# Performance work log

Measured on AMD Instinct MI355X. Metric: run time of the kernel, lower is better.

Reference implementation:

```python
import jax, jax.numpy as jnp
import numpy as np

B, S, H, NSPAN = 16, 1024, 768, 5
NEG_INF = -1e9


def setup_inputs() -> dict:
    key = jax.random.key(0)
    k1, k2, k3, k4, k5, k6 = jax.random.split(key, 6)
    hidden = jax.random.normal(k1, (B, S, H), dtype=jnp.float32)
    full_emb = jax.random.normal(k2, (B, H), dtype=jnp.float32)
    # nn.Linear weights [out,in] per span head, plus biases and queries
    attn_W = jax.random.normal(k3, (NSPAN, H, H), dtype=jnp.float32) / np.sqrt(H)
    attn_b = jax.random.normal(k4, (NSPAN, H), dtype=jnp.float32) * 0.02
    attn_q = jax.random.uniform(k5, (NSPAN, H), dtype=jnp.float32)  # torch.rand init
    spans = jnp.sort(jax.random.randint(k6, (B, NSPAN, 2), 0, S), axis=-1)
    return {"hidden": hidden, "full_emb": full_emb, "attn_W": attn_W,
            "attn_b": attn_b, "attn_q": attn_q, "spans": spans}


def reference(hidden, full_emb, attn_W, attn_b, attn_q, spans):
    b, s, h = hidden.shape
    starts = spans[..., 0]            # [B,J]
    ends = spans[..., 1]              # [B,J]
    pos = jnp.arange(s)
    mask = (pos[None, None, :] >= starts[..., None]) & (pos[None, None, :] < ends[..., None])  # [B,J,S]
    count = mask.sum(-1)              # [B,J]
    fmask = mask.astype(hidden.dtype)

    # mean pool over each span (zeros when start==end)
    mean = jnp.einsum('bjs,bsh->bjh', fmask, hidden) / jnp.maximum(count, 1).astype(hidden.dtype)[..., None]

    # learned attention pool: tanh(Linear_j(words)), scores vs query_j, softmax over span
    proj = jnp.tanh(jnp.einsum('bsh,joh->bjso', hidden, attn_W) + attn_b[None, :, None, :])  # [B,J,S,H]
    scores = jnp.einsum('jo,bjso->bjs', attn_q, proj)
    scores = jnp.where(mask, scores, NEG_INF)  # max-subtraction in original is a detached shift => identical
    alphas = jax.nn.softmax(scores, axis=-1)
    att = jnp.einsum('bjs,bsh->bjh', alphas, hidden)

    nonempty = (count > 0)[..., None]
    mean = jnp.where(nonempty, mean, 0.0)
    att = jnp.where(nonempty, att, 0.0)

    span_reps = jnp.concatenate([mean, att], axis=-1)          # [B,J,2H], order [mean_j, att_j]
    final = jnp.concatenate([span_reps.reshape(b, -1), full_emb], axis=-1)  # [B, J*2H + H]
    return (final, full_emb)
```

## Files before the change

### kernel.cpp

```cpp
#include <hip/hip_runtime.h>

#define BB 16
#define SS 1024
#define HH 768
#define JJ 5
#define WHJ (HH*HH)
#define RIDX_J (BB*SS)
#define NSEG 8

typedef __attribute__((ext_vector_type(4))) _Float16 h4_t;
typedef __attribute__((ext_vector_type(8))) _Float16 h8_t;
typedef __attribute__((ext_vector_type(4))) float f32x4;

#define WH_HALVES (JJ*HH*HH)
#define WH_BYTES  (WH_HALVES*2)
#define HID_HALVES (BB*SS*HH)
#define HID_BYTES (HID_HALVES*2)
#define SC_FLOATS (BB*JJ*SS)
#define SC_BYTES  (SC_FLOATS*4)
#define RIDX_BYTES (JJ*RIDX_J*4)
#define FINAL_W   (JJ*2*HH + HH)
#define OUT2_OFF  (BB*FINAL_W)

#define NB_CONV (HID_HALVES/4/256)
#define NB_IDX  (JJ*BB)
#define NB_TAIL (BB)

__global__ void k_convert(const float* __restrict__ W, const float* __restrict__ hidden,
                          const float* __restrict__ full_emb, const int* __restrict__ spans,
                          _Float16* __restrict__ Wh, _Float16* __restrict__ Hh,
                          float* __restrict__ scores, int* __restrict__ ridx,
                          int* __restrict__ meta, float* __restrict__ out)
{
    const int bid = blockIdx.x, tid = threadIdx.x;
    __shared__ int cnts[BB];

    if (bid < NB_CONV) {
        int i = bid * 256 + tid;
        {
            float4 v = *(const float4*)(hidden + (size_t)i * 4);
            h4_t hv = { (_Float16)v.x, (_Float16)v.y, (_Float16)v.z, (_Float16)v.w };
            *(h4_t*)(Hh + (size_t)i * 4) = hv;
        }
        if (i < WH_HALVES / 4) {
            float4 v = *(const float4*)(W + (size_t)i * 4);
            h4_t hv = { (_Float16)v.x, (_Float16)v.y, (_Float16)v.z, (_Float16)v.w };
            *(h4_t*)(Wh + (size_t)i * 4) = hv;
        }
        if (i < SC_FLOATS) scores[i] = 0.f;

        if (bid == 0 && tid < 64) {
            int l = tid, l15 = l & 15, lg = l >> 4;
            h8_t a1, b1, a2, b2;
#pragma unroll
            for (int jj = 0; jj < 8; ++jj) {
                int k1 = (jj & 3) + 4 * lg + 16 * (jj >> 2);
                int k2 = jj + 8 * lg;
                a1[jj] = (_Float16)(float)((l15 * 31 + k1 * 17) % 13 - 6);
                b1[jj] = (_Float16)(float)((k1 * 7 + l15 * 5) % 11 - 5);
                a2[jj] = (_Float16)(float)((l15 * 31 + k2 * 17) % 13 - 6);
                b2[jj] = (_Float16)(float)((k2 * 7 + l15 * 5) % 11 - 5);
            }
            f32x4 z = { 0.f, 0.f, 0.f, 0.f };
            f32x4 c1 = __builtin_amdgcn_mfma_f32_16x16x32_f16(a1, b1, z, 0, 0, 0);
            f32x4 c2 = __builtin_amdgcn_mfma_f32_16x16x32_f16(a2, b2, z, 0, 0, 0);
            int ok1 = 1, ok2 = 1;
#pragma unroll
            for (int r = 0; r < 4; ++r) {
                int row = lg * 4 + r;
                float ref = 0.f;
                for (int k = 0; k < 32; ++k)
                    ref += (float)((row * 31 + k * 17) % 13 - 6) *
                           (float)((k * 7 + l15 * 5) % 11 - 5);
                ok1 &= (c1[r] == ref);
                ok2 &= (c2[r] == ref);
            }
            int all1 = __all(ok1);
            int all2 = __all(ok2);
            if (l == 0) meta[5] = all1 ? 1 : (all2 ? 2 : 0);
        }
        return;
    }

    if (bid < NB_CONV + NB_IDX) {
        const int seg = bid - NB_CONV;
        const int j = seg / BB, b = seg % BB;
        if (tid < BB) {
            int st = spans[(tid * JJ + j) * 2 + 0];
            int en = spans[(tid * JJ + j) * 2 + 1];
            cnts[tid] = (en > st) ? (en - st) : 0;
        }
        __syncthreads();
        if (b == 0 && tid == 0) {
            int tot = 0;
            for (int b2 = 0; b2 < BB; ++b2) tot += cnts[b2];
            meta[j] = tot;
        }
        int off = 0;
        for (int b2 = 0; b2 < b; ++b2) off += cnts[b2];
        const int st = spans[(b * JJ + j) * 2 + 0];
        const int cnt = cnts[b];
        const int base = j * RIDX_J + off;
        for (int i = tid; i < cnt; i += 256)
            ridx[base + i] = b * SS + st + i;
        return;
    }

    {
        const int b = bid - NB_CONV - NB_IDX;
        float* ob = out + (size_t)b * FINAL_W;
        for (int h = tid; h < JJ * 2 * HH; h += 256) ob[h] = 0.f;
        for (int h = tid; h < HH; h += 256) {
            float v = full_emb[b * HH + h];
            ob[JJ * 2 * HH + h] = v;
            out[OUT2_OFF + b * HH + h] = v;
        }
    }
}

__device__ __forceinline__ void epilogue(
    f32x4 (&acc)[4][4], const float* qv, const float* bvec, float* scores,
    const int* s_ridx, float* s_red, int j, int nblk, int valid_rows,
    int tid, int wm, int wn, int lg, int l15)
{
    float qn[4], bn[4];
#pragma unroll
    for (int c = 0; c < 4; ++c) {
        int col = nblk * 128 + wn * 64 + c * 16 + l15;
        qn[c] = qv[col];
        bn[c] = bvec[col];
    }
#pragma unroll
    for (int a = 0; a < 4; ++a) {
#pragma unroll
        for (int rr = 0; rr < 4; ++rr) {
            float ssum = 0.f;
#pragma unroll
            for (int c = 0; c < 4; ++c) {
                float yv = acc[a][c][rr] + bn[c];
                yv = fminf(fmaxf(yv, -15.f), 15.f);
                float e = __expf(2.f * yv);
                ssum += qn[c] * ((e - 1.f) / (e + 1.f));
            }
#pragma unroll
            for (int off = 1; off < 16; off <<= 1)
                ssum += __shfl_xor(ssum, off, 64);
            if (l15 == 0)
                s_red[(wm * 2 + wn) * 64 + a * 16 + lg * 4 + rr] = ssum;
        }
    }
    __syncthreads();
    if (tid < valid_rows) {
        int wm2 = tid >> 6, rl = tid & 63;
        float v = s_red[(wm2 * 2) * 64 + rl] + s_red[(wm2 * 2 + 1) * 64 + rl];
        int gidx = s_ridx[tid];
        atomicAdd(&scores[(gidx >> 10) * (JJ * SS) + j * SS + (gidx & 1023)], v);
    }
}

template<int LAYOUT>
__device__ __forceinline__ void scores_reg(
    const _Float16* __restrict__ Hh, const _Float16* __restrict__ wj,
    const float* __restrict__ qv, const float* __restrict__ bvec,
    float* __restrict__ scores, const int* s_ridx,
    _Float16* Alds, _Float16* Blds, float* s_red,
    int j, int nblk, int valid_rows, int tid)
{
    const int r  = tid >> 1, hh = tid & 1;
    const int mf = r >> 4,  mr = r & 15;
    const _Float16* ap = Hh + (size_t)s_ridx[r] * HH + hh * 32;
    const _Float16* bp = wj + (size_t)(nblk * 128 + r) * HH + hh * 32;

    const int wave = tid >> 6, lane = tid & 63;
    const int l15 = lane & 15, lg = lane >> 4;
    const int wm = wave >> 1, wn = wave & 1;

    f32x4 acc[4][4];
#pragma unroll
    for (int a = 0; a < 4; ++a)
#pragma unroll
        for (int c = 0; c < 4; ++c) acc[a][c] = (f32x4){0.f, 0.f, 0.f, 0.f};

    for (int ks = 0; ks < 12; ++ks) {
        h8_t av[4], bv4[4];
        const _Float16* a0 = ap + ks * 64;
        const _Float16* b0 = bp + ks * 64;
#pragma unroll
        for (int g2 = 0; g2 < 4; ++g2) {
            av[g2]  = *(const h8_t*)(a0 + g2 * 8);
            bv4[g2] = *(const h8_t*)(b0 + g2 * 8);
        }
        __syncthreads();
        if (LAYOUT == 2) {
#pragma unroll
            for (int g2 = 0; g2 < 4; ++g2) {
                int c = ((mf * 2 + hh) * 4 + g2) * 16 + mr;
                *(h8_t*)(Alds + c * 8) = av[g2];
                *(h8_t*)(Blds + c * 8) = bv4[g2];
            }
        } else {
#pragma unroll
            for (int g2 = 0; g2 < 4; ++g2) {
                int k0a = g2 * 8, k0b = g2 * 8 + 4;
                int ga = (k0a & 15) >> 2, ja = (k0a >> 4) << 2;
                int gb = (k0b & 15) >> 2, jb = (k0b >> 4) << 2;
                int cA = ((mf * 2 + hh) * 4 + ga) * 16 + mr;
                int cB = ((mf * 2 + hh) * 4 + gb) * 16 + mr;
                h8_t x = av[g2];
                h4_t alo = { x[0], x[1], x[2], x[3] };
                h4_t ahi = { x[4], x[5], x[6], x[7] };
                *(h4_t*)(Alds + cA * 8 + ja) = alo;
                *(h4_t*)(Alds + cB * 8 + jb) = ahi;
                h8_t y = bv4[g2];
                h4_t blo = { y[0], y[1], y[2], y[3] };
                h4_t bhi = { y[4], y[5], y[6], y[7] };
                *(h4_t*)(Blds + cA * 8 + ja) = blo;
                *(h4_t*)(Blds + cB * 8 + jb) = bhi;
            }
        }
        __syncthreads();
#pragma unroll
        for (int ks2 = 0; ks2 < 2; ++ks2) {
            h8_t af[4], bf[4];
#pragma unroll
            for (int f = 0; f < 4; ++f) {
                int ca = (((wm * 4 + f) * 2 + ks2) * 4 + lg) * 16 + l15;
                af[f] = *(const h8_t*)(Alds + ca * 8);
                int cb = (((wn * 4 + f) * 2 + ks2) * 4 + lg) * 16 + l15;
                bf[f] = *(const h8_t*)(Blds + cb * 8);
            }
#pragma unroll
            for (int a = 0; a < 4; ++a)
#pragma unroll
                for (int c = 0; c < 4; ++c)
                    acc[a][c] = __builtin_amdgcn_mfma_f32_16x16x32_f16(
                        af[a], bf[c], acc[a][c], 0, 0, 0);
        }
    }
    epilogue(acc, qv, bvec, scores, s_ridx, s_red, j, nblk, valid_rows,
             tid, wm, wn, lg, l15);
}

__global__ __launch_bounds__(256, 4) void k_scores(
    const _Float16* __restrict__ Hh, const _Float16* __restrict__ Wh,
    const float* __restrict__ attn_b, const float* __restrict__ attn_q,
    float* __restrict__ scores, const int* __restrict__ ridx,
    const int* __restrict__ meta)
{
    const int tile = blockIdx.x, nblk = blockIdx.y, j = blockIdx.z;
    const int Mj = meta[j];
    const int rows_base = tile * 128;
    if (rows_base >= Mj) return;
    const int valid_rows = min(128, Mj - rows_base);

    __shared__ __align__(16) _Float16 Alds[1024 * 8];
    __shared__ __align__(16) _Float16 Blds[1024 * 8];
    __shared__ int   s_ridx[128];
    __shared__ float s_red[256];

    const int tid = threadIdx.x;
    if (tid < 128)
        s_ridx[tid] = ridx[j * RIDX_J + rows_base + min(tid, valid_rows - 1)];
    __syncthreads();

    const _Float16* wj = Wh + (size_t)j * WHJ;
    const float* qv = attn_q + j * HH;
    const float* bv = attn_b + j * HH;

    if (meta[5] == 2)
        scores_reg<2>(Hh, wj, qv, bv, scores, s_ridx, Alds, Blds, s_red,
                      j, nblk, valid_rows, tid);
    else
        scores_reg<1>(Hh, wj, qv, bv, scores, s_ridx, Alds, Blds, s_red,
                      j, nblk, valid_rows, tid);
}

__global__ __launch_bounds__(256) void k_pool(
    const _Float16* __restrict__ Hh, const float* __restrict__ scores,
    const int* __restrict__ spans, float* __restrict__ out)
{
    const int bj = blockIdx.x, seg = blockIdx.y;
    const int b = bj / JJ, j = bj % JJ;
    const int start = spans[bj * 2 + 0];
    const int end   = spans[bj * 2 + 1];
    const int count = end - start;
    if (count <= 0) return;

    const int tid = threadIdx.x;
    const float* sc = scores + bj * SS;
    __shared__ float red[8];
    __shared__ float wl[SS / NSEG + 1];

    float lm = -3.0e38f;
    for (int s = start + tid; s < end; s += 256) lm = fmaxf(lm, sc[s]);
#pragma unroll
    for (int off = 32; off > 0; off >>= 1) lm = fmaxf(lm, __shfl_xor(lm, off, 64));
    int wid = tid >> 6, lane = tid & 63;
    if (lane == 0) red[wid] = lm;
    __syncthreads();
    float m = fmaxf(fmaxf(red[0], red[1]), fmaxf(red[2], red[3]));

    float ld = 0.f;
    for (int s = start + tid; s < end; s += 256) ld += __expf(sc[s] - m);
#pragma unroll
    for (int off = 32; off > 0; off >>= 1) ld += __shfl_xor(ld, off, 64);
    if (lane == 0) red[4 + wid] = ld;
    __syncthreads();
    float inv_d = 1.f / (red[4] + red[5] + red[6] + red[7]);

    const int i0 = start + (count * seg) / NSEG;
    const int i1 = start + (count * (seg + 1)) / NSEG;
    for (int s = i0 + tid; s < i1; s += 256)
        wl[s - i0] = __expf(sc[s] - m) * inv_d;
    __syncthreads();

    if (tid < 192) {
        float am[4] = {0.f, 0.f, 0.f, 0.f}, aa[4] = {0.f, 0.f, 0.f, 0.f};
        const _Float16* hp = Hh + (size_t)b * SS * HH + tid * 4;
        const int n = i1 - i0;
        int i = 0;
        for (; i + 4 <= n; i += 4) {
            h4_t v0 = *(const h4_t*)(hp + (size_t)(i0 + i + 0) * HH);
            h4_t v1 = *(const h4_t*)(hp + (size_t)(i0 + i + 1) * HH);
            h4_t v2 = *(const h4_t*)(hp + (size_t)(i0 + i + 2) * HH);
            h4_t v3 = *(const h4_t*)(hp + (size_t)(i0 + i + 3) * HH);
            float w0 = wl[i], w1 = wl[i + 1], w2 = wl[i + 2], w3 = wl[i + 3];
#pragma unroll
            for (int c = 0; c < 4; ++c) {
                float x0 = (float)v0[c], x1 = (float)v1[c];
                float x2 = (float)v2[c], x3 = (float)v3[c];
                am[c] += (x0 + x1) + (x2 + x3);
                aa[c] += (w0 * x0 + w1 * x1) + (w2 * x2 + w3 * x3);
            }
        }
        for (; i < n; ++i) {
            h4_t v = *(const h4_t*)(hp + (size_t)(i0 + i) * HH);
            float w = wl[i];
#pragma unroll
            for (int c = 0; c < 4; ++c) {
                float x = (float)v[c];
                am[c] += x;
                aa[c] += w * x;
            }
        }
        float inv = 1.f / (float)count;
        float* fin = out + (size_t)b * FINAL_W + j * (2 * HH);
#pragma unroll
        for (int c = 0; c < 4; ++c) {
            atomicAdd(&fin[tid * 4 + c], am[c] * inv);
            atomicAdd(&fin[HH + tid * 4 + c], aa[c]);
        }
    }
}

extern "C" void kernel_launch(void* const* d_in, const int* in_sizes, int n_in,
                              void* d_out, int out_size, void* d_ws, size_t ws_size,
                              hipStream_t stream)
{
    const float* hidden   = (const float*)d_in[0];
    const float* full_emb = (const float*)d_in[1];
    const float* attn_W   = (const float*)d_in[2];
    const float* attn_b   = (const float*)d_in[3];
    const float* attn_q   = (const float*)d_in[4];
    const int*   spans    = (const int*)d_in[5];
    float* out = (float*)d_out;

    char* ws = (char*)d_ws;
    _Float16* Wh  = (_Float16*)ws;
    _Float16* Hh  = (_Float16*)(ws + WH_BYTES);
    float* scores = (float*)(ws + WH_BYTES + HID_BYTES);
    int*   ridx   = (int*)(ws + WH_BYTES + HID_BYTES + SC_BYTES);
    int*   meta   = (int*)(ws + WH_BYTES + HID_BYTES + SC_BYTES + RIDX_BYTES);

    k_convert<<<NB_CONV + NB_IDX + NB_TAIL, 256, 0, stream>>>(
        attn_W, hidden, full_emb, spans, Wh, Hh, scores, ridx, meta, out);
    k_scores<<<dim3(RIDX_J / 128, HH / 128, JJ), 256, 0, stream>>>(
        Hh, Wh, attn_b, attn_q, scores, ridx, meta);
    k_pool<<<dim3(BB * JJ, NSEG), 256, 0, stream>>>(Hh, scores, spans, out);
}
```

Measured before the change: 117.3 us.

## Enlarge score GEMM tile to 256 rows with 512-thread blocks

The scores kernel now handles 256 gathered hidden rows per block instead of 128, using 512 threads arranged as a 4x2 grid of waves. Each block now loads the 128-column weight tile once and shares it across twice as many rows, which halves weight-tile reloads from global memory. The B-loading pattern is reworked so four threads load each weight row, 16 halves each, and write it into the same LDS layout as before. In exchange, LDS use per block grows, fewer blocks fit per CU, and partially filled tiles waste more work when a span head has few rows.

```diff
diff --git a/kernel.cpp b/kernel.cpp
--- a/kernel.cpp
+++ b/kernel.cpp
@@ -169,7 +169,10 @@
     const int r  = tid >> 1, hh = tid & 1;
     const int mf = r >> 4,  mr = r & 15;
     const _Float16* ap = Hh + (size_t)s_ridx[r] * HH + hh * 32;
-    const _Float16* bp = wj + (size_t)(nblk * 128 + r) * HH + hh * 32;
+
+    const int rb = tid >> 2, q = tid & 3;
+    const int mfB = rb >> 4, mrB = rb & 15;
+    const _Float16* bp = wj + (size_t)(nblk * 128 + rb) * HH + q * 16;
 
     const int wave = tid >> 6, lane = tid & 63;
     const int l15 = lane & 15, lg = lane >> 4;
@@ -182,21 +185,27 @@
         for (int c = 0; c < 4; ++c) acc[a][c] = (f32x4){0.f, 0.f, 0.f, 0.f};
 
     for (int ks = 0; ks < 12; ++ks) {
-        h8_t av[4], bv4[4];
+        h8_t av[4], bv2[2];
         const _Float16* a0 = ap + ks * 64;
         const _Float16* b0 = bp + ks * 64;
 #pragma unroll
-        for (int g2 = 0; g2 < 4; ++g2) {
-            av[g2]  = *(const h8_t*)(a0 + g2 * 8);
-            bv4[g2] = *(const h8_t*)(b0 + g2 * 8);
-        }
+        for (int g2 = 0; g2 < 4; ++g2)
+            av[g2] = *(const h8_t*)(a0 + g2 * 8);
+#pragma unroll
+        for (int u = 0; u < 2; ++u)
+            bv2[u] = *(const h8_t*)(b0 + u * 8);
         __syncthreads();
         if (LAYOUT == 2) {
 #pragma unroll
             for (int g2 = 0; g2 < 4; ++g2) {
                 int c = ((mf * 2 + hh) * 4 + g2) * 16 + mr;
                 *(h8_t*)(Alds + c * 8) = av[g2];
-                *(h8_t*)(Blds + c * 8) = bv4[g2];
+            }
+#pragma unroll
+            for (int u = 0; u < 2; ++u) {
+                int ka = q * 16 + u * 8;
+                int c = ((mfB * 2 + (ka >> 5)) * 4 + ((ka & 31) >> 3)) * 16 + mrB;
+                *(h8_t*)(Blds + c * 8) = bv2[u];
             }
         } else {
 #pragma unroll
@@ -211,11 +220,19 @@
                 h4_t ahi = { x[4], x[5], x[6], x[7] };
                 *(h4_t*)(Alds + cA * 8 + ja) = alo;
                 *(h4_t*)(Alds + cB * 8 + jb) = ahi;
-                h8_t y = bv4[g2];
-                h4_t blo = { y[0], y[1], y[2], y[3] };
-                h4_t bhi = { y[4], y[5], y[6], y[7] };
-                *(h4_t*)(Blds + cA * 8 + ja) = blo;
-                *(h4_t*)(Blds + cB * 8 + jb) = bhi;
+            }
+#pragma unroll
+            for (int u = 0; u < 2; ++u) {
+                h8_t y = bv2[u];
+#pragma unroll
+                for (int v = 0; v < 2; ++v) {
+                    int k = q * 16 + u * 8 + v * 4;
+                    int kk = k & 31;
+                    int g = (kk & 15) >> 2, j0 = (kk >> 4) << 2;
+                    int c = ((mfB * 2 + (k >> 5)) * 4 + g) * 16 + mrB;
+                    h4_t hv = { y[v * 4 + 0], y[v * 4 + 1], y[v * 4 + 2], y[v * 4 + 3] };
+                    *(h4_t*)(Blds + c * 8 + j0) = hv;
+                }
             }
         }
         __syncthreads();
@@ -241,7 +258,7 @@
              tid, wm, wn, lg, l15);
 }
 
-__global__ __launch_bounds__(256, 4) void k_scores(
+__global__ __launch_bounds__(512, 6) void k_scores(
     const _Float16* __restrict__ Hh, const _Float16* __restrict__ Wh,
     const float* __restrict__ attn_b, const float* __restrict__ attn_q,
     float* __restrict__ scores, const int* __restrict__ ridx,
@@ -249,17 +266,17 @@
 {
     const int tile = blockIdx.x, nblk = blockIdx.y, j = blockIdx.z;
     const int Mj = meta[j];
-    const int rows_base = tile * 128;
+    const int rows_base = tile * 256;
     if (rows_base >= Mj) return;
-    const int valid_rows = min(128, Mj - rows_base);
-
-    __shared__ __align__(16) _Float16 Alds[1024 * 8];
+    const int valid_rows = min(256, Mj - rows_base);
+
+    __shared__ __align__(16) _Float16 Alds[2048 * 8];
     __shared__ __align__(16) _Float16 Blds[1024 * 8];
-    __shared__ int   s_ridx[128];
-    __shared__ float s_red[256];
+    __shared__ int   s_ridx[256];
+    __shared__ float s_red[512];
 
     const int tid = threadIdx.x;
-    if (tid < 128)
+    if (tid < 256)
         s_ridx[tid] = ridx[j * RIDX_J + rows_base + min(tid, valid_rows - 1)];
     __syncthreads();
 
@@ -374,7 +391,7 @@
 
     k_convert<<<NB_CONV + NB_IDX + NB_TAIL, 256, 0, stream>>>(
         attn_W, hidden, full_emb, spans, Wh, Hh, scores, ridx, meta, out);
-    k_scores<<<dim3(RIDX_J / 128, HH / 128, JJ), 256, 0, stream>>>(
+    k_scores<<<dim3(RIDX_J / 256, HH / 128, JJ), 512, 0, stream>>>(
         Hh, Wh, attn_b, attn_q, scores, ridx, meta);
     k_pool<<<dim3(BB * JJ, NSEG), 256, 0, stream>>>(Hh, scores, spans, out);
 }
```

Measured after the change: 389.3 us. 232% more time.
